# Kernel optimization log

Measured on AMD Instinct MI355X. Metric: run time of the kernel, lower is better.

## Reference

```python
import jax, jax.numpy as jnp
import numpy as np

DN = ('NCDHW', 'OIDHW', 'NCDHW')  # conv dimension numbers for 3D conv in torch layout
EPS = 1e-14


def setup_inputs() -> dict:
    key = jax.random.key(0)
    k1, k2 = jax.random.split(key)
    # xs: [B, C, D, H, W]
    xs = jax.random.normal(k1, (16, 128, 24, 24, 24), dtype=jnp.float32)
    # feature_vectors (prototypes): [num_features, C, w_1, h_1, L_1]
    feature_vectors = jax.random.normal(k2, (128, 128, 3, 3, 3), dtype=jnp.float32)
    return {"xs": xs, "feature_vectors": feature_vectors}


def reference(xs, feature_vectors):
    F_, C, kd, kh, kw = feature_vectors.shape
    # ||x_patch||^2: the original convolves xs**2 with all-ones weights of shape
    # [F, C, kd, kh, kw], producing F identical channels. We compute a single
    # sum-pool channel (same math) and let broadcasting supply the F channels.
    ones = jnp.ones((1, C, kd, kh, kw), dtype=xs.dtype)
    xs_squared_l2 = jax.lax.conv_general_dilated(
        xs * xs, ones, window_strides=(1, 1, 1), padding='VALID',
        dimension_numbers=DN)  # [B, 1, D', H', W']
    # ||p||^2 per prototype: [F, 1, 1, 1]
    ps_squared_l2 = jnp.sum(feature_vectors * feature_vectors,
                            axis=(1, 2, 3, 4)).reshape(-1, 1, 1, 1)
    # <x_patch, p>: the real weighted conv. [B, F, D', H', W']
    xs_conv = jax.lax.conv_general_dilated(
        xs, feature_vectors, window_strides=(1, 1, 1), padding='VALID',
        dimension_numbers=DN)
    distance = xs_squared_l2 + ps_squared_l2 - 2.0 * xs_conv
    return jnp.sqrt(jnp.abs(distance) + EPS)
```

## Files before the change

### kernel.cpp

```cpp
#include <hip/hip_runtime.h>
#include <hip/hip_bf16.h>

typedef __attribute__((ext_vector_type(8))) __bf16 bf16x8;
typedef __attribute__((ext_vector_type(4))) float f32x4;

#define B_   16
#define C_   128
#define DIM  24
#define F_   128
#define OD   22
#define OS   (OD*OD*OD)
#define SPB  (DIM*DIM*DIM)
#define K_   3456
#define M_   (B_*OS)
#define OUTN (B_*F_*OS)

__device__ __forceinline__ void async16(const void* g, void* l) {
  __builtin_amdgcn_global_load_lds(
      (const __attribute__((address_space(1))) unsigned int*)g,
      (__attribute__((address_space(3))) unsigned int*)l, 16, 0, 0);
}

__global__ void prep_x(const float* __restrict__ xs, __bf16* __restrict__ xt,
                       float* __restrict__ s1) {
  __shared__ float tile[C_ * DIM];
  const int blk = blockIdx.x;
  const int y = blk % DIM;
  const int t2 = blk / DIM;
  const int z = t2 % DIM;
  const int b = t2 / DIM;
  const float* src = xs + (size_t)b * C_ * SPB + z * (DIM * DIM) + y * DIM;
  for (int it = 0; it < (C_ * DIM) / 256; ++it) {
    int idx = it * 256 + threadIdx.x;
    int c = idx / DIM, x = idx - c * DIM;
    tile[c * DIM + x] = src[(size_t)c * SPB + x];
  }
  __syncthreads();
  size_t obase = (size_t)blk * DIM * C_;
  for (int it = 0; it < (C_ * DIM) / 256; ++it) {
    int idx = it * 256 + threadIdx.x;
    int c = idx & (C_ - 1), x = idx >> 7;
    xt[obase + (size_t)x * C_ + c] = (__bf16)tile[c * DIM + x];
  }
  if (threadIdx.x < DIM) {
    float s = 0.f;
    for (int c = 0; c < C_; ++c) {
      float v = tile[c * DIM + threadIdx.x];
      s += v * v;
    }
    s1[blk * DIM + threadIdx.x] = s;
  }
}

__global__ void prep_w(const float* __restrict__ fv, __bf16* __restrict__ Wt,
                       float* __restrict__ psq) {
  const int f = blockIdx.x;
  const float* src = fv + (size_t)f * K_;
  float part = 0.f;
  for (int idx = threadIdx.x; idx < K_; idx += 256) {
    int c = idx & 127, off = idx >> 7;
    float v = src[c * 27 + off];
    part += v * v;
    Wt[(size_t)f * K_ + idx] = (__bf16)v;
  }
  for (int o = 32; o > 0; o >>= 1) part += __shfl_down(part, o, 64);
  __shared__ float red[4];
  int w = threadIdx.x >> 6, l = threadIdx.x & 63;
  if (l == 0) red[w] = part;
  __syncthreads();
  if (threadIdx.x == 0) psq[f] = red[0] + red[1] + red[2] + red[3];
}

__global__ void pool_sq(const float* __restrict__ s1, float* __restrict__ xsq) {
  int i = blockIdx.x * 256 + threadIdx.x;
  if (i >= M_) return;
  int ow = i % OD;
  int t = i / OD;
  int oh = t % OD; t /= OD;
  int od = t % OD;
  int b = t / OD;
  const float* p = s1 + ((b * DIM + od) * DIM + oh) * DIM + ow;
  float s = 0.f;
#pragma unroll
  for (int dz = 0; dz < 3; ++dz)
#pragma unroll
    for (int dy = 0; dy < 3; ++dy)
#pragma unroll
      for (int dx = 0; dx < 3; ++dx)
        s += p[dz * 576 + dy * 24 + dx];
  xsq[i] = s;
}

__global__ __launch_bounds__(256) void l2gemm(
    const __bf16* __restrict__ xt, const __bf16* __restrict__ Wt,
    const float* __restrict__ xsq, const float* __restrict__ psq,
    float* __restrict__ out) {
  __shared__ __align__(16) __bf16 Wl[128 * 64];
  __shared__ __align__(16) __bf16 Pl[128 * 64];
  const int t = threadIdx.x;
  const int l = t & 63, w = t >> 6;
  const int quad = l >> 4, lan = l & 15;
  const int e = t & 7, r0 = t >> 3;
  const int mt = blockIdx.x;

  int sb[4];
#pragma unroll
  for (int p = 0; p < 4; ++p) {
    int m = mt * 128 + r0 + 32 * p;
    int b = m / OS;
    int s = m - b * OS;
    int od = s / (OD * OD);
    int s2 = s - od * (OD * OD);
    int oh = s2 / OD;
    int ow = s2 - oh * OD;
    sb[p] = b * SPB + od * 576 + oh * 24 + ow;
  }

  f32x4 acc[4][4];
#pragma unroll
  for (int i = 0; i < 4; ++i)
#pragma unroll
    for (int n = 0; n < 4; ++n) acc[i][n] = (f32x4){0.f, 0.f, 0.f, 0.f};

  const int wm = (w >> 1) * 64;
  const int wn = (w & 1) * 64;
  __bf16* wl_base = &Wl[(w * 8) * 64];
  __bf16* pl_base = &Pl[(w * 8) * 64];

#pragma unroll 1
  for (int kt = 0; kt < 54; ++kt) {
    int off = kt >> 1;
    int dz = off / 9;
    int rem = off - dz * 9;
    int dy = rem / 3;
    int dx = rem - dy * 3;
    int doff = dz * 576 + dy * 24 + dx;
    int c0 = (kt & 1) << 6;
    __syncthreads();
#pragma unroll
    for (int p = 0; p < 4; ++p) {
      const __bf16* gp = xt + (((size_t)(sb[p] + doff)) << 7) + c0 + e * 8;
      async16(gp, pl_base + (size_t)(32 * p) * 64);
      const __bf16* gw = Wt + (size_t)(r0 + 32 * p) * K_ + kt * 64 + e * 8;
      async16(gw, wl_base + (size_t)(32 * p) * 64);
    }
    __syncthreads();
#pragma unroll
    for (int kk = 0; kk < 2; ++kk) {
      bf16x8 a[4], bb[4];
#pragma unroll
      for (int i = 0; i < 4; ++i)
        a[i] = *(const bf16x8*)&Wl[(wm + i * 16 + lan) * 64 + kk * 32 + quad * 8];
#pragma unroll
      for (int n = 0; n < 4; ++n)
        bb[n] = *(const bf16x8*)&Pl[(wn + n * 16 + lan) * 64 + kk * 32 + quad * 8];
#pragma unroll
      for (int i = 0; i < 4; ++i)
#pragma unroll
        for (int n = 0; n < 4; ++n)
          acc[i][n] = __builtin_amdgcn_mfma_f32_16x16x32_bf16(a[i], bb[n],
                                                              acc[i][n], 0, 0, 0);
    }
  }

  int mb[4];
  float xv[4];
#pragma unroll
  for (int n = 0; n < 4; ++n) {
    int m = mt * 128 + wn + n * 16 + lan;
    int b = m / OS;
    int s = m - b * OS;
    mb[n] = b * (F_ * OS) + s;
    xv[n] = xsq[m];
  }
#pragma unroll
  for (int i = 0; i < 4; ++i) {
#pragma unroll
    for (int r = 0; r < 4; ++r) {
      int f = wm + i * 16 + quad * 4 + r;
      float pq = psq[f];
#pragma unroll
      for (int n = 0; n < 4; ++n) {
        float d = xv[n] + pq - 2.0f * acc[i][n][r];
        out[mb[n] + f * OS] = sqrtf(fabsf(d) + 1e-14f);
      }
    }
  }
}

__global__ void l2conv_direct(const float* __restrict__ xs,
                              const float* __restrict__ fv,
                              float* __restrict__ out) {
  int i = blockIdx.x * 256 + threadIdx.x;
  if (i >= OUTN) return;
  int s = i % OS;
  int t2 = i / OS;
  int f = t2 & 127;
  int b = t2 >> 7;
  int od = s / (OD * OD);
  int s2 = s - od * (OD * OD);
  int oh = s2 / OD;
  int ow = s2 - oh * OD;
  const float* xp = xs + (size_t)b * C_ * SPB + od * 576 + oh * 24 + ow;
  const float* wp = fv + (size_t)f * K_;
  float dot = 0.f, xq = 0.f, pq = 0.f;
  for (int c = 0; c < C_; ++c) {
    const float* xpc = xp + (size_t)c * SPB;
    const float* wpc = wp + c * 27;
#pragma unroll
    for (int o = 0; o < 27; ++o) {
      int dz = o / 9;
      int ry = o - dz * 9;
      int dy = ry / 3;
      int dx = ry - dy * 3;
      float xv = xpc[dz * 576 + dy * 24 + dx];
      float wv = wpc[o];
      dot += xv * wv;
      xq += xv * xv;
      pq += wv * wv;
    }
  }
  out[i] = sqrtf(fabsf(xq + pq - 2.f * dot) + 1e-14f);
}

extern "C" void kernel_launch(void* const* d_in, const int* in_sizes, int n_in,
                              void* d_out, int out_size, void* d_ws,
                              size_t ws_size, hipStream_t stream) {
  const float* xs = (const float*)d_in[0];
  const float* fv = (const float*)d_in[1];
  float* out = (float*)d_out;

  const size_t xt_b  = (size_t)B_ * SPB * C_ * 2;
  const size_t wt_b  = (size_t)F_ * K_ * 2;
  const size_t s1_b  = (size_t)B_ * SPB * 4;
  const size_t xsq_b = (size_t)M_ * 4;
  const size_t psq_b = 512;
  if (ws_size < xt_b + wt_b + s1_b + xsq_b + psq_b) {
    l2conv_direct<<<(OUTN + 255) / 256, 256, 0, stream>>>(xs, fv, out);
    return;
  }
  char* p = (char*)d_ws;
  __bf16* xt = (__bf16*)p;          p += xt_b;
  __bf16* Wt = (__bf16*)p;          p += wt_b;
  float*  s1 = (float*)p;           p += s1_b;
  float*  xsq = (float*)p;          p += xsq_b;
  float*  psq = (float*)p;

  prep_x<<<B_ * DIM * DIM, 256, 0, stream>>>(xs, xt, s1);
  prep_w<<<F_, 256, 0, stream>>>(fv, Wt, psq);
  pool_sq<<<(M_ + 255) / 256, 256, 0, stream>>>(s1, xsq);
  l2gemm<<<M_ / 128, 256, 0, stream>>>(xt, Wt, xsq, psq, out);
}
```

Before: 455.2 us.

## Swizzle GEMM LDS layout and vectorize prep_x transpose with padded tiles

```diff
diff --git a/kernel.cpp b/kernel.cpp
--- a/kernel.cpp
+++ b/kernel.cpp
@@ -2,6 +2,7 @@
 #include <hip/hip_bf16.h>
 
 typedef __attribute__((ext_vector_type(8))) __bf16 bf16x8;
+typedef __attribute__((ext_vector_type(2))) __bf16 bf16x2;
 typedef __attribute__((ext_vector_type(4))) float f32x4;
 
 #define B_   16
@@ -21,47 +22,64 @@
       (__attribute__((address_space(3))) unsigned int*)l, 16, 0, 0);
 }
 
-__global__ void prep_x(const float* __restrict__ xs, __bf16* __restrict__ xt,
-                       float* __restrict__ s1) {
-  __shared__ float tile[C_ * DIM];
+__global__ __launch_bounds__(256) void prep_x(const float* __restrict__ xs,
+                                              __bf16* __restrict__ xt,
+                                              float* __restrict__ s1) {
+  __shared__ float tile[C_ * 97];
+  __shared__ float red[192];
   const int blk = blockIdx.x;
-  const int y = blk % DIM;
-  const int t2 = blk / DIM;
+  const int yg = blk % 6;
+  const int t2 = blk / 6;
   const int z = t2 % DIM;
   const int b = t2 / DIM;
-  const float* src = xs + (size_t)b * C_ * SPB + z * (DIM * DIM) + y * DIM;
-  for (int it = 0; it < (C_ * DIM) / 256; ++it) {
-    int idx = it * 256 + threadIdx.x;
-    int c = idx / DIM, x = idx - c * DIM;
-    tile[c * DIM + x] = src[(size_t)c * SPB + x];
-  }
-  __syncthreads();
-  size_t obase = (size_t)blk * DIM * C_;
-  for (int it = 0; it < (C_ * DIM) / 256; ++it) {
-    int idx = it * 256 + threadIdx.x;
-    int c = idx & (C_ - 1), x = idx >> 7;
-    xt[obase + (size_t)x * C_ + c] = (__bf16)tile[c * DIM + x];
-  }
-  if (threadIdx.x < DIM) {
+  const int t = threadIdx.x;
+  const float* src = xs + (size_t)b * C_ * SPB + z * (DIM * DIM) + yg * 96;
+  for (int it = 0; it < 12; ++it) {
+    int idx = it * 256 + t;
+    int c = idx / 24, f4 = idx - c * 24;
+    const float4 v = *(const float4*)(src + (size_t)c * SPB + f4 * 4);
+    float* d = &tile[c * 97 + f4 * 4];
+    d[0] = v.x; d[1] = v.y; d[2] = v.z; d[3] = v.w;
+  }
+  __syncthreads();
+  size_t obase = ((size_t)b * SPB + z * (DIM * DIM) + yg * 96) * C_;
+  for (int it = 0; it < 24; ++it) {
+    int idx = it * 256 + t;
+    int c2 = idx & 63, x = idx >> 6;
+    bf16x2 v;
+    v[0] = (__bf16)tile[(2 * c2) * 97 + x];
+    v[1] = (__bf16)tile[(2 * c2 + 1) * 97 + x];
+    *(bf16x2*)&xt[obase + (size_t)x * C_ + 2 * c2] = v;
+  }
+  if (t < 192) {
+    int g = t / 96, p = t - g * 96;
     float s = 0.f;
-    for (int c = 0; c < C_; ++c) {
-      float v = tile[c * DIM + threadIdx.x];
+    for (int c = g; c < C_; c += 2) {
+      float v = tile[c * 97 + p];
       s += v * v;
     }
-    s1[blk * DIM + threadIdx.x] = s;
-  }
+    red[g * 96 + p] = s;
+  }
+  __syncthreads();
+  if (t < 96)
+    s1[((size_t)b * SPB + z * (DIM * DIM) + yg * 96) + t] = red[t] + red[96 + t];
 }
 
 __global__ void prep_w(const float* __restrict__ fv, __bf16* __restrict__ Wt,
                        float* __restrict__ psq) {
+  __shared__ float tile[K_];
   const int f = blockIdx.x;
   const float* src = fv + (size_t)f * K_;
   float part = 0.f;
   for (int idx = threadIdx.x; idx < K_; idx += 256) {
+    float v = src[idx];
+    tile[idx] = v;
+    part += v * v;
+  }
+  __syncthreads();
+  for (int idx = threadIdx.x; idx < K_; idx += 256) {
     int c = idx & 127, off = idx >> 7;
-    float v = src[c * 27 + off];
-    part += v * v;
-    Wt[(size_t)f * K_ + idx] = (__bf16)v;
+    Wt[(size_t)f * K_ + idx] = (__bf16)tile[c * 27 + off];
   }
   for (int o = 32; o > 0; o >>= 1) part += __shfl_down(part, o, 64);
   __shared__ float red[4];
@@ -101,6 +119,7 @@
   const int l = t & 63, w = t >> 6;
   const int quad = l >> 4, lan = l & 15;
   const int e = t & 7, r0 = t >> 3;
+  const int esw = (e ^ (r0 & 7)) * 8;
   const int mt = blockIdx.x;
 
   int sb[4];
@@ -139,21 +158,22 @@
     __syncthreads();
 #pragma unroll
     for (int p = 0; p < 4; ++p) {
-      const __bf16* gp = xt + (((size_t)(sb[p] + doff)) << 7) + c0 + e * 8;
+      const __bf16* gp = xt + (((size_t)(sb[p] + doff)) << 7) + c0 + esw;
       async16(gp, pl_base + (size_t)(32 * p) * 64);
-      const __bf16* gw = Wt + (size_t)(r0 + 32 * p) * K_ + kt * 64 + e * 8;
+      const __bf16* gw = Wt + (size_t)(r0 + 32 * p) * K_ + kt * 64 + esw;
       async16(gw, wl_base + (size_t)(32 * p) * 64);
     }
     __syncthreads();
 #pragma unroll
     for (int kk = 0; kk < 2; ++kk) {
       bf16x8 a[4], bb[4];
+      const int swz = (((kk * 4 + quad) ^ (lan & 7))) * 8;
 #pragma unroll
       for (int i = 0; i < 4; ++i)
-        a[i] = *(const bf16x8*)&Wl[(wm + i * 16 + lan) * 64 + kk * 32 + quad * 8];
+        a[i] = *(const bf16x8*)&Wl[(wm + i * 16 + lan) * 64 + swz];
 #pragma unroll
       for (int n = 0; n < 4; ++n)
-        bb[n] = *(const bf16x8*)&Pl[(wn + n * 16 + lan) * 64 + kk * 32 + quad * 8];
+        bb[n] = *(const bf16x8*)&Pl[(wn + n * 16 + lan) * 64 + swz];
 #pragma unroll
       for (int i = 0; i < 4; ++i)
 #pragma unroll
@@ -246,7 +266,7 @@
   float*  xsq = (float*)p;          p += xsq_b;
   float*  psq = (float*)p;
 
-  prep_x<<<B_ * DIM * DIM, 256, 0, stream>>>(xs, xt, s1);
+  prep_x<<<B_ * DIM * DIM / 4, 256, 0, stream>>>(xs, xt, s1);
   prep_w<<<F_, 256, 0, stream>>>(fv, Wt, psq);
   pool_sq<<<(M_ + 255) / 256, 256, 0, stream>>>(s1, xsq);
   l2gemm<<<M_ / 128, 256, 0, stream>>>(xt, Wt, xsq, psq, out);
```

After: 410.1 us. 9.9% less time.
